# Performance work log

Hardware: AMD Instinct MI355X
Metric: run time of the kernel (lower is better)

## Reference

```python
import jax, jax.numpy as jnp
import numpy as np

B, T, S, D, V = 8, 64, 512, 512, 50000


def setup_inputs() -> dict:
    key = jax.random.key(0)
    k1, k2, k3, k4, k5 = jax.random.split(key, 5)
    x = jax.random.normal(k1, (B, T, D), dtype=jnp.float32)
    attn_dist = jax.random.normal(k2, (B, T, S), dtype=jnp.float32)
    enc_batch_extend_vocab = jax.random.randint(k3, (B, S), 0, V, dtype=jnp.int64)
    W_proj = jax.random.normal(k4, (D, V), dtype=jnp.float32) * (1.0 / np.sqrt(D))
    b_proj = jnp.zeros((V,), dtype=jnp.float32)
    W_pgen = jax.random.normal(k5, (D, 1), dtype=jnp.float32) * (1.0 / np.sqrt(D))
    b_pgen = jnp.zeros((1,), dtype=jnp.float32)
    return {"x": x, "attn_dist": attn_dist,
            "enc_batch_extend_vocab": enc_batch_extend_vocab,
            "W_proj": W_proj, "b_proj": b_proj,
            "W_pgen": W_pgen, "b_pgen": b_pgen}


def reference(x, attn_dist, enc_batch_extend_vocab, W_proj, b_proj, W_pgen, b_pgen):
    # pointer-generator head, temp=1, beam_search=False
    temp = 1.0
    # p_gen gate: [B, T, 1]
    alpha = jax.nn.sigmoid(jnp.einsum('btd,de->bte', x, W_pgen) + b_pgen)
    # vocab projection + softmax: [B, T, V]
    logit = jnp.einsum('btd,dv->btv', x, W_proj) + b_proj
    vocab_dist = jax.nn.softmax(logit / temp, axis=2)
    vocab_dist_ = alpha * vocab_dist
    # copy distribution over source positions: [B, T, S]
    attn = jax.nn.softmax(attn_dist / temp, axis=-1)
    attn_ = (1.0 - alpha) * attn
    # scatter_add copy probs into vocab dim (index broadcast over T)
    b_idx = jnp.arange(B)[:, None, None]        # [B,1,1]
    t_idx = jnp.arange(T)[None, :, None]        # [1,T,1]
    v_idx = enc_batch_extend_vocab[:, None, :]  # [B,1,S]
    merged = vocab_dist_.at[b_idx, t_idx, v_idx].add(attn_)
    return jnp.log(merged)
```

## Files before the change

### kernel.cpp

```cpp
#include <hip/hip_runtime.h>
#include <math.h>
#include <stdint.h>

#define B_ 8
#define T_ 64
#define S_ 512
#define D_ 512
#define V_ 50000
#define VP_ 50176
#define M_ (B_*T_)
#define ROWB_ ((size_t)V_ * 4)

typedef __bf16 bf16_t;
typedef bf16_t bf16x8 __attribute__((ext_vector_type(8)));
typedef float  f32x4  __attribute__((ext_vector_type(4)));

__device__ inline float blk_sum(float v, float* sm) {
    #pragma unroll
    for (int o = 32; o > 0; o >>= 1) v += __shfl_down(v, o);
    int lane = threadIdx.x & 63, wid = threadIdx.x >> 6;
    __syncthreads();
    if (lane == 0) sm[wid] = v;
    __syncthreads();
    return sm[0] + sm[1] + sm[2] + sm[3];
}

__device__ inline float blk_max(float v, float* sm) {
    #pragma unroll
    for (int o = 32; o > 0; o >>= 1) v = fmaxf(v, __shfl_down(v, o));
    int lane = threadIdx.x & 63, wid = threadIdx.x >> 6;
    __syncthreads();
    if (lane == 0) sm[wid] = v;
    __syncthreads();
    return fmaxf(fmaxf(sm[0], sm[1]), fmaxf(sm[2], sm[3]));
}

__device__ inline void unpack8(uint4 u, float f[8]) {
    uint32_t w0 = u.x, w1 = u.y, w2 = u.z, w3 = u.w;
    f[0] = __uint_as_float(w0 << 16); f[1] = __uint_as_float(w0 & 0xffff0000u);
    f[2] = __uint_as_float(w1 << 16); f[3] = __uint_as_float(w1 & 0xffff0000u);
    f[4] = __uint_as_float(w2 << 16); f[5] = __uint_as_float(w2 & 0xffff0000u);
    f[6] = __uint_as_float(w3 << 16); f[7] = __uint_as_float(w3 & 0xffff0000u);
}

__global__ __launch_bounds__(256) void k1_alpha_attn(
    const float* __restrict__ x, const float* __restrict__ attn_dist,
    const float* __restrict__ W_pgen, const float* __restrict__ b_pgen,
    float* __restrict__ logalpha_out, float* __restrict__ attn_out, bf16_t* __restrict__ xb)
{
    __shared__ float sm[4];
    int row = blockIdx.x;
    int tid = threadIdx.x;

    float2 xv = reinterpret_cast<const float2*>(x + (size_t)row * D_)[tid];
    float2 wv = reinterpret_cast<const float2*>(W_pgen)[tid];
    union { bf16_t h[2]; uint32_t u; } pk;
    pk.h[0] = (bf16_t)xv.x; pk.h[1] = (bf16_t)xv.y;
    reinterpret_cast<uint32_t*>(xb + (size_t)row * D_)[tid] = pk.u;

    float dot = blk_sum(xv.x * wv.x + xv.y * wv.y, sm);
    float alpha = 1.f / (1.f + expf(-(dot + b_pgen[0])));
    if (tid == 0) logalpha_out[row] = logf(alpha);

    float a0 = attn_dist[(size_t)row * S_ + tid];
    float a1 = attn_dist[(size_t)row * S_ + tid + 256];
    float mx = blk_max(fmaxf(a0, a1), sm);
    float e0 = expf(a0 - mx), e1 = expf(a1 - mx);
    float s = blk_sum(e0 + e1, sm);
    float scale = (1.f - alpha) / s;
    attn_out[(size_t)row * S_ + tid]       = e0 * scale;
    attn_out[(size_t)row * S_ + tid + 256] = e1 * scale;
}

__global__ __launch_bounds__(256) void conv_wt(const float* __restrict__ W, bf16_t* __restrict__ Wt)
{
    __shared__ float tile[64][65];
    int v0 = blockIdx.x * 64;
    int k0 = blockIdx.y * 64;
    int tid = threadIdx.x;
    #pragma unroll
    for (int p = 0; p < 4; p++) {
        int kl = (tid >> 4) + p * 16;
        int v  = v0 + (tid & 15) * 4;
        float4 val = make_float4(0.f, 0.f, 0.f, 0.f);
        if (v < V_)
            val = *reinterpret_cast<const float4*>(&W[(size_t)(k0 + kl) * V_ + v]);
        tile[kl][(tid & 15) * 4 + 0] = val.x;
        tile[kl][(tid & 15) * 4 + 1] = val.y;
        tile[kl][(tid & 15) * 4 + 2] = val.z;
        tile[kl][(tid & 15) * 4 + 3] = val.w;
    }
    __syncthreads();
    #pragma unroll
    for (int p = 0; p < 2; p++) {
        int vl = (tid >> 3) + p * 32;
        int kc = (tid & 7) * 8;
        union { bf16_t h[8]; uint4 u; } pk;
        #pragma unroll
        for (int j = 0; j < 8; j++) pk.h[j] = (bf16_t)tile[kc + j][vl];
        *reinterpret_cast<uint4*>(&Wt[(size_t)(v0 + vl) * D_ + k0 + kc]) = pk.u;
    }
}

#define GBM 128
#define GBN 128
#define GBK 32

__global__ __launch_bounds__(256) void k2_mfma(
    const bf16_t* __restrict__ A, const bf16_t* __restrict__ Wt,
    const float* __restrict__ bias, char* __restrict__ outB)
{
    __shared__ bf16_t As[GBM][GBK];
    __shared__ bf16_t Bs[GBN][GBK];
    int tid  = threadIdx.x;
    int lane = tid & 63;
    int w    = tid >> 6;
    int wm   = w >> 1, wn = w & 1;
    int bn = blockIdx.x * GBN;
    int bm = blockIdx.y * GBM;

    f32x4 acc[4][4] = {};

    for (int k0 = 0; k0 < D_; k0 += GBK) {
        #pragma unroll
        for (int i = 0; i < 2; i++) {
            int e = (w * 2 + i) * 512 + lane * 8;
            int r = e >> 5, c = e & 31;
            const bf16_t* g = &A[(size_t)(bm + r) * D_ + k0 + c];
            __builtin_amdgcn_global_load_lds(
                (const __attribute__((address_space(1))) void*)g,
                (__attribute__((address_space(3))) void*)&As[(w * 2 + i) * 16][0],
                16, 0, 0);
        }
        #pragma unroll
        for (int i = 0; i < 2; i++) {
            int e = (w * 2 + i) * 512 + lane * 8;
            int n = e >> 5, c = e & 31;
            const bf16_t* g = &Wt[(size_t)(bn + n) * D_ + k0 + c];
            __builtin_amdgcn_global_load_lds(
                (const __attribute__((address_space(1))) void*)g,
                (__attribute__((address_space(3))) void*)&Bs[(w * 2 + i) * 16][0],
                16, 0, 0);
        }
        asm volatile("s_waitcnt vmcnt(0)" ::: "memory");
        __syncthreads();

        bf16x8 af[4], bfr[4];
        int kb = (lane >> 4) * 8;
        #pragma unroll
        for (int mi = 0; mi < 4; mi++)
            af[mi] = *reinterpret_cast<const bf16x8*>(&As[wm * 64 + mi * 16 + (lane & 15)][kb]);
        #pragma unroll
        for (int ni = 0; ni < 4; ni++)
            bfr[ni] = *reinterpret_cast<const bf16x8*>(&Bs[wn * 64 + ni * 16 + (lane & 15)][kb]);
        #pragma unroll
        for (int mi = 0; mi < 4; mi++)
            #pragma unroll
            for (int ni = 0; ni < 4; ni++)
                acc[mi][ni] = __builtin_amdgcn_mfma_f32_16x16x32_bf16(af[mi], bfr[ni], acc[mi][ni], 0, 0, 0);
        __syncthreads();
    }

    int cm = bm + wm * 64, cn = bn + wn * 64;
    #pragma unroll
    for (int ni = 0; ni < 4; ni++) {
        int n = cn + ni * 16 + (lane & 15);
        float bv = (n < V_) ? bias[n] : 0.f;
        #pragma unroll
        for (int mi = 0; mi < 4; mi++) {
            int rbase = cm + mi * 16 + (lane >> 4) * 4;
            #pragma unroll
            for (int r = 0; r < 4; r++) {
                bf16_t val = (bf16_t)(acc[mi][ni][r] + bv);
                *reinterpret_cast<bf16_t*>(outB + (size_t)(rbase + r) * ROWB_ + 2 * (size_t)n) = val;
            }
        }
    }
}

__global__ __launch_bounds__(512) void k5a_owner(const int* __restrict__ idx, int* __restrict__ owner_g)
{
    __shared__ int ids[S_];
    int b = blockIdx.x;
    int s = threadIdx.x;
    ids[s] = idx[b * S_ + s];
    __syncthreads();
    int v = ids[s], o = s;
    for (int s2 = 0; s2 < s; s2++) if (ids[s2] == v) { o = s2; break; }
    owner_g[b * S_ + s] = o;
}

#define CHUNK_ 2048
#define NCH_ ((V_ + CHUNK_ - 1) / CHUNK_)

__global__ __launch_bounds__(256) void k345_final(
    char* __restrict__ outB, const float* __restrict__ attn_, const int* __restrict__ idx,
    const int* __restrict__ owner_g, const float* __restrict__ logalpha)
{
    __shared__ float att[S_];
    __shared__ int own[S_], ids[S_];
    __shared__ float smm[4], sms[4];
    int row = blockIdx.x;
    int b = row >> 6;
    int tid = threadIdx.x;
    int lane = tid & 63, wid = tid >> 6;

    for (int s = tid; s < S_; s += 256) {
        att[s] = attn_[(size_t)row * S_ + s];
        own[s] = owner_g[b * S_ + s];
        ids[s] = idx[b * S_ + s];
    }

    const uint4* L4 = reinterpret_cast<const uint4*>(outB + (size_t)row * ROWB_);
    float m = -INFINITY, se = 0.f;
    for (int i = tid; i < V_ / 8; i += 256) {
        uint4 u = L4[i];
        float f[8]; unpack8(u, f);
        float m8 = fmaxf(fmaxf(fmaxf(f[0], f[1]), fmaxf(f[2], f[3])),
                         fmaxf(fmaxf(f[4], f[5]), fmaxf(f[6], f[7])));
        float mn = fmaxf(m, m8);
        se = se * __expf(m - mn)
           + __expf(f[0] - mn) + __expf(f[1] - mn) + __expf(f[2] - mn) + __expf(f[3] - mn)
           + __expf(f[4] - mn) + __expf(f[5] - mn) + __expf(f[6] - mn) + __expf(f[7] - mn);
        m = mn;
    }
    #pragma unroll
    for (int o = 32; o > 0; o >>= 1) {
        float m2 = __shfl_down(m, o);
        float s2 = __shfl_down(se, o);
        float mn = fmaxf(m, m2);
        if (mn == -INFINITY) { se = 0.f; }
        else se = se * __expf(m - mn) + s2 * __expf(m2 - mn);
        m = mn;
    }
    __syncthreads();
    if (lane == 0) { smm[wid] = m; sms[wid] = se; }
    __syncthreads();
    float M = smm[0], Ssum = sms[0];
    #pragma unroll
    for (int wv = 1; wv < 4; wv++) {
        float m2 = smm[wv], s2 = sms[wv];
        float mn = fmaxf(M, m2);
        if (mn != -INFINITY) Ssum = Ssum * __expf(M - mn) + s2 * __expf(m2 - mn);
        M = mn;
    }
    float logden = M + logf(Ssum);
    float c_ = logalpha[row] - logden;

    for (int s = tid; s < S_; s += 256)
        if (own[s] != s) atomicAdd(&att[own[s]], att[s]);
    __syncthreads();

    const ushort* Lrow = reinterpret_cast<const ushort*>(outB + (size_t)row * ROWB_);
    float* frow = reinterpret_cast<float*>(outB + (size_t)row * ROWB_);
    for (int c = NCH_ - 1; c >= 0; c--) {
        int i0 = c * CHUNK_ + tid * 8;
        uint4 u = make_uint4(0, 0, 0, 0);
        bool act = (i0 + 8 <= V_);
        if (act) u = *reinterpret_cast<const uint4*>(Lrow + i0);
        __syncthreads();
        if (act) {
            float f[8]; unpack8(u, f);
            float4 lo = make_float4(f[0] + c_, f[1] + c_, f[2] + c_, f[3] + c_);
            float4 hi = make_float4(f[4] + c_, f[5] + c_, f[6] + c_, f[7] + c_);
            *reinterpret_cast<float4*>(frow + i0)     = lo;
            *reinterpret_cast<float4*>(frow + i0 + 4) = hi;
        }
        __syncthreads();
    }

    for (int s = tid; s < S_; s += 256) {
        if (own[s] == s) {
            int v = ids[s];
            frow[v] = logf(expf(frow[v]) + att[s]);
        }
    }
}

#define BM 64
#define BN 64
#define BK 16
__global__ __launch_bounds__(256) void k2_gemm(
    const float* __restrict__ A, const float* __restrict__ W,
    const float* __restrict__ bias, float* __restrict__ C)
{
    __shared__ float As2[BK][BM + 1];
    __shared__ float Bs2[BK][BN + 1];
    int bn = blockIdx.x * BN;
    int bm = blockIdx.y * BM;
    int tid = threadIdx.x;
    int tx = tid & 15;
    int ty = tid >> 4;
    bool full_n = (bn + BN <= V_);
    float acc[4][4] = {};
    for (int k0 = 0; k0 < D_; k0 += BK) {
        {
            int i = tid * 4;
            int row = i >> 4, col = i & 15;
            const float4 av = *reinterpret_cast<const float4*>(&A[(size_t)(bm + row) * D_ + k0 + col]);
            As2[col + 0][row] = av.x; As2[col + 1][row] = av.y;
            As2[col + 2][row] = av.z; As2[col + 3][row] = av.w;
        }
        {
            int i = tid * 4;
            int row = i >> 6, col = i & 63;
            int gn = bn + col;
            if (full_n) {
                const float4 bv = *reinterpret_cast<const float4*>(&W[(size_t)(k0 + row) * V_ + gn]);
                Bs2[row][col + 0] = bv.x; Bs2[row][col + 1] = bv.y;
                Bs2[row][col + 2] = bv.z; Bs2[row][col + 3] = bv.w;
            } else {
                #pragma unroll
                for (int j = 0; j < 4; j++)
                    Bs2[row][col + j] = (gn + j < V_) ? W[(size_t)(k0 + row) * V_ + gn + j] : 0.f;
            }
        }
        __syncthreads();
        #pragma unroll
        for (int kk = 0; kk < BK; kk++) {
            float a[4], b[4];
            #pragma unroll
            for (int i = 0; i < 4; i++) a[i] = As2[kk][ty * 4 + i];
            #pragma unroll
            for (int j = 0; j < 4; j++) b[j] = Bs2[kk][tx + j * 16];
            #pragma unroll
            for (int i = 0; i < 4; i++)
                #pragma unroll
                for (int j = 0; j < 4; j++)
                    acc[i][j] += a[i] * b[j];
        }
        __syncthreads();
    }
    #pragma unroll
    for (int i = 0; i < 4; i++) {
        int m = bm + ty * 4 + i;
        #pragma unroll
        for (int j = 0; j < 4; j++) {
            int n = bn + tx + j * 16;
            if (n < V_) C[(size_t)m * V_ + n] = acc[i][j] + bias[n];
        }
    }
}

__global__ __launch_bounds__(256) void k3_stats(const float* __restrict__ C, float* __restrict__ logden)
{
    __shared__ float smm[4], sms[4];
    int row = blockIdx.x;
    const float4* p = reinterpret_cast<const float4*>(C + (size_t)row * V_);
    float m = -INFINITY, s = 0.f;
    for (int i = threadIdx.x; i < V_ / 4; i += 256) {
        float4 v = p[i];
        float m4 = fmaxf(fmaxf(v.x, v.y), fmaxf(v.z, v.w));
        if (m4 > m) { s *= expf(m - m4); m = m4; }
        s += expf(v.x - m) + expf(v.y - m) + expf(v.z - m) + expf(v.w - m);
    }
    #pragma unroll
    for (int o = 32; o > 0; o >>= 1) {
        float m2 = __shfl_down(m, o);
        float s2 = __shfl_down(s, o);
        float mn = fmaxf(m, m2);
        s = s * expf(m - mn) + s2 * expf(m2 - mn);
        m = mn;
    }
    int lane = threadIdx.x & 63, wid = threadIdx.x >> 6;
    if (lane == 0) { smm[wid] = m; sms[wid] = s; }
    __syncthreads();
    if (threadIdx.x == 0) {
        float M = smm[0], S = sms[0];
        #pragma unroll
        for (int wv = 1; wv < 4; wv++) {
            float m2 = smm[wv], s2 = sms[wv];
            float mn = fmaxf(M, m2);
            S = S * expf(M - mn) + s2 * expf(m2 - mn);
            M = mn;
        }
        logden[row] = M + logf(S);
    }
}

__global__ __launch_bounds__(256) void k4_scale(
    float* __restrict__ C, const float* __restrict__ logalpha, const float* __restrict__ logden)
{
    int row = blockIdx.y;
    int i = blockIdx.x * 256 + threadIdx.x;
    if (i >= V_ / 4) return;
    float c_ = logalpha[row] - logden[row];
    float4* p = reinterpret_cast<float4*>(C + (size_t)row * V_) + i;
    float4 v = *p;
    v.x += c_; v.y += c_; v.z += c_; v.w += c_;
    *p = v;
}

__global__ __launch_bounds__(256) void k5_scatter_log(
    float* __restrict__ C, const float* __restrict__ attn_, const int* __restrict__ idx,
    const int* __restrict__ owner_g)
{
    __shared__ float att[S_];
    __shared__ int own[S_], ids[S_];
    int row = blockIdx.x;
    int b = row >> 6;
    int tid = threadIdx.x;
    for (int s = tid; s < S_; s += 256) {
        att[s] = attn_[(size_t)row * S_ + s];
        own[s] = owner_g[b * S_ + s];
        ids[s] = idx[b * S_ + s];
    }
    __syncthreads();
    for (int s = tid; s < S_; s += 256)
        if (own[s] != s) atomicAdd(&att[own[s]], att[s]);
    __syncthreads();
    for (int s = tid; s < S_; s += 256) {
        if (own[s] == s) {
            int v = ids[s];
            float* p = &C[(size_t)row * V_ + v];
            *p = logf(expf(*p) + att[s]);
        }
    }
}

extern "C" void kernel_launch(void* const* d_in, const int* in_sizes, int n_in,
                              void* d_out, int out_size, void* d_ws, size_t ws_size,
                              hipStream_t stream) {
    const float* x         = (const float*)d_in[0];
    const float* attn_dist = (const float*)d_in[1];
    const int*   ebev      = (const int*)  d_in[2];
    const float* W_proj    = (const float*)d_in[3];
    const float* b_proj    = (const float*)d_in[4];
    const float* W_pgen    = (const float*)d_in[5];
    const float* b_pgen    = (const float*)d_in[6];
    float* out = (float*)d_out;
    char*  outB = (char*)d_out;

    float*  logalpha = (float*)d_ws;
    float*  logden   = logalpha + M_;
    float*  attn_    = logden + M_;
    int*    owner    = (int*)(attn_ + (size_t)B_ * T_ * S_);
    bf16_t* xb       = (bf16_t*)(owner + (size_t)B_ * S_);
    bf16_t* Wt       = xb + (size_t)M_ * D_;
    size_t need = (size_t)(2 * M_ + B_ * T_ * S_ + B_ * S_) * 4
                + (size_t)M_ * D_ * 2 + (size_t)VP_ * D_ * 2;

    k1_alpha_attn<<<M_, 256, 0, stream>>>(x, attn_dist, W_pgen, b_pgen, logalpha, attn_, xb);
    k5a_owner<<<B_, 512, 0, stream>>>(ebev, owner);

    if (ws_size >= need) {
        dim3 gt(VP_ / 64, D_ / 64);
        conv_wt<<<gt, 256, 0, stream>>>(W_proj, Wt);

        dim3 g2(VP_ / GBN, M_ / GBM);
        k2_mfma<<<g2, 256, 0, stream>>>(xb, Wt, b_proj, outB);

        k345_final<<<M_, 256, 0, stream>>>(outB, attn_, ebev, owner, logalpha);
    } else {
        dim3 g2((V_ + BN - 1) / BN, M_ / BM);
        k2_gemm<<<g2, 256, 0, stream>>>(x, W_proj, b_proj, out);
        k3_stats<<<M_, 256, 0, stream>>>(out, logden);
        dim3 g4((V_ / 4 + 255) / 256, M_);
        k4_scale<<<g4, 256, 0, stream>>>(out, logalpha, logden);
        k5_scatter_log<<<M_, 256, 0, stream>>>(out, attn_, ebev, owner);
    }
}
```

Measured before the change: 172.1 us.

## Merge prep kernels into one launch and double-buffer MFMA GEMM LDS tiles

Three preprocessing kernels (weight transpose/convert to bf16, alpha/attention softmax with x conversion, and the duplicate-index owner computation) are merged into one launch that dispatches work by block index. This removes two launch gaps and lets the small tasks run alongside the large conversion. The bf16 MFMA GEMM now uses two LDS buffers, issuing the next k-tile's global-to-LDS loads before computing the current tile, so the sync per k-step overlaps load latency with MFMA work. LDS use doubles and the owner loop now runs over 256 threads with two iterations each.

```diff
diff --git a/kernel.cpp b/kernel.cpp
--- a/kernel.cpp
+++ b/kernel.cpp
@@ -43,75 +43,90 @@
     f[6] = __uint_as_float(w3 << 16); f[7] = __uint_as_float(w3 & 0xffff0000u);
 }
 
-__global__ __launch_bounds__(256) void k1_alpha_attn(
+#define CONVB_ (784 * 8)
+
+__global__ __launch_bounds__(256) void kprep(
+    const float* __restrict__ W, bf16_t* __restrict__ Wt,
     const float* __restrict__ x, const float* __restrict__ attn_dist,
     const float* __restrict__ W_pgen, const float* __restrict__ b_pgen,
-    float* __restrict__ logalpha_out, float* __restrict__ attn_out, bf16_t* __restrict__ xb)
-{
-    __shared__ float sm[4];
-    int row = blockIdx.x;
+    float* __restrict__ logalpha_out, float* __restrict__ attn_out, bf16_t* __restrict__ xb,
+    const int* __restrict__ idx, int* __restrict__ owner_g)
+{
+    __shared__ float tile[64][65];
+    int bid = blockIdx.x;
     int tid = threadIdx.x;
 
-    float2 xv = reinterpret_cast<const float2*>(x + (size_t)row * D_)[tid];
-    float2 wv = reinterpret_cast<const float2*>(W_pgen)[tid];
-    union { bf16_t h[2]; uint32_t u; } pk;
-    pk.h[0] = (bf16_t)xv.x; pk.h[1] = (bf16_t)xv.y;
-    reinterpret_cast<uint32_t*>(xb + (size_t)row * D_)[tid] = pk.u;
-
-    float dot = blk_sum(xv.x * wv.x + xv.y * wv.y, sm);
-    float alpha = 1.f / (1.f + expf(-(dot + b_pgen[0])));
-    if (tid == 0) logalpha_out[row] = logf(alpha);
-
-    float a0 = attn_dist[(size_t)row * S_ + tid];
-    float a1 = attn_dist[(size_t)row * S_ + tid + 256];
-    float mx = blk_max(fmaxf(a0, a1), sm);
-    float e0 = expf(a0 - mx), e1 = expf(a1 - mx);
-    float s = blk_sum(e0 + e1, sm);
-    float scale = (1.f - alpha) / s;
-    attn_out[(size_t)row * S_ + tid]       = e0 * scale;
-    attn_out[(size_t)row * S_ + tid + 256] = e1 * scale;
-}
-
-__global__ __launch_bounds__(256) void conv_wt(const float* __restrict__ W, bf16_t* __restrict__ Wt)
-{
-    __shared__ float tile[64][65];
-    int v0 = blockIdx.x * 64;
-    int k0 = blockIdx.y * 64;
-    int tid = threadIdx.x;
-    #pragma unroll
-    for (int p = 0; p < 4; p++) {
-        int kl = (tid >> 4) + p * 16;
-        int v  = v0 + (tid & 15) * 4;
-        float4 val = make_float4(0.f, 0.f, 0.f, 0.f);
-        if (v < V_)
-            val = *reinterpret_cast<const float4*>(&W[(size_t)(k0 + kl) * V_ + v]);
-        tile[kl][(tid & 15) * 4 + 0] = val.x;
-        tile[kl][(tid & 15) * 4 + 1] = val.y;
-        tile[kl][(tid & 15) * 4 + 2] = val.z;
-        tile[kl][(tid & 15) * 4 + 3] = val.w;
-    }
-    __syncthreads();
-    #pragma unroll
-    for (int p = 0; p < 2; p++) {
-        int vl = (tid >> 3) + p * 32;
-        int kc = (tid & 7) * 8;
-        union { bf16_t h[8]; uint4 u; } pk;
+    if (bid < CONVB_) {
+        int v0 = (bid % 784) * 64;
+        int k0 = (bid / 784) * 64;
         #pragma unroll
-        for (int j = 0; j < 8; j++) pk.h[j] = (bf16_t)tile[kc + j][vl];
-        *reinterpret_cast<uint4*>(&Wt[(size_t)(v0 + vl) * D_ + k0 + kc]) = pk.u;
+        for (int p = 0; p < 4; p++) {
+            int kl = (tid >> 4) + p * 16;
+            int v  = v0 + (tid & 15) * 4;
+            float4 val = make_float4(0.f, 0.f, 0.f, 0.f);
+            if (v < V_)
+                val = *reinterpret_cast<const float4*>(&W[(size_t)(k0 + kl) * V_ + v]);
+            tile[kl][(tid & 15) * 4 + 0] = val.x;
+            tile[kl][(tid & 15) * 4 + 1] = val.y;
+            tile[kl][(tid & 15) * 4 + 2] = val.z;
+            tile[kl][(tid & 15) * 4 + 3] = val.w;
+        }
+        __syncthreads();
+        #pragma unroll
+        for (int p = 0; p < 2; p++) {
+            int vl = (tid >> 3) + p * 32;
+            int kc = (tid & 7) * 8;
+            union { bf16_t h[8]; uint4 u; } pk;
+            #pragma unroll
+            for (int j = 0; j < 8; j++) pk.h[j] = (bf16_t)tile[kc + j][vl];
+            *reinterpret_cast<uint4*>(&Wt[(size_t)(v0 + vl) * D_ + k0 + kc]) = pk.u;
+        }
+    } else if (bid < CONVB_ + M_) {
+        float* sm = &tile[0][0];
+        int row = bid - CONVB_;
+
+        float2 xv = reinterpret_cast<const float2*>(x + (size_t)row * D_)[tid];
+        float2 wv = reinterpret_cast<const float2*>(W_pgen)[tid];
+        union { bf16_t h[2]; uint32_t u; } pk;
+        pk.h[0] = (bf16_t)xv.x; pk.h[1] = (bf16_t)xv.y;
+        reinterpret_cast<uint32_t*>(xb + (size_t)row * D_)[tid] = pk.u;
+
+        float dot = blk_sum(xv.x * wv.x + xv.y * wv.y, sm);
+        float alpha = 1.f / (1.f + expf(-(dot + b_pgen[0])));
+        if (tid == 0) logalpha_out[row] = logf(alpha);
+
+        float a0 = attn_dist[(size_t)row * S_ + tid];
+        float a1 = attn_dist[(size_t)row * S_ + tid + 256];
+        float mx = blk_max(fmaxf(a0, a1), sm);
+        float e0 = expf(a0 - mx), e1 = expf(a1 - mx);
+        float s = blk_sum(e0 + e1, sm);
+        float scale = (1.f - alpha) / s;
+        attn_out[(size_t)row * S_ + tid]       = e0 * scale;
+        attn_out[(size_t)row * S_ + tid + 256] = e1 * scale;
+    } else {
+        int* ids = reinterpret_cast<int*>(&tile[0][0]);
+        int b = bid - (CONVB_ + M_);
+        for (int s = tid; s < S_; s += 256) ids[s] = idx[b * S_ + s];
+        __syncthreads();
+        for (int s = tid; s < S_; s += 256) {
+            int v = ids[s], o = s;
+            for (int s2 = 0; s2 < s; s2++) if (ids[s2] == v) { o = s2; break; }
+            owner_g[b * S_ + s] = o;
+        }
     }
 }
 
 #define GBM 128
 #define GBN 128
 #define GBK 32
+#define NT2_ (D_/GBK)
 
 __global__ __launch_bounds__(256) void k2_mfma(
     const bf16_t* __restrict__ A, const bf16_t* __restrict__ Wt,
     const float* __restrict__ bias, char* __restrict__ outB)
 {
-    __shared__ bf16_t As[GBM][GBK];
-    __shared__ bf16_t Bs[GBN][GBK];
+    __shared__ bf16_t As0[GBM][GBK], As1[GBM][GBK];
+    __shared__ bf16_t Bs0[GBN][GBK], Bs1[GBN][GBK];
     int tid  = threadIdx.x;
     int lane = tid & 63;
     int w    = tid >> 6;
@@ -121,45 +136,60 @@
 
     f32x4 acc[4][4] = {};
 
-    for (int k0 = 0; k0 < D_; k0 += GBK) {
-        #pragma unroll
-        for (int i = 0; i < 2; i++) {
-            int e = (w * 2 + i) * 512 + lane * 8;
-            int r = e >> 5, c = e & 31;
-            const bf16_t* g = &A[(size_t)(bm + r) * D_ + k0 + c];
-            __builtin_amdgcn_global_load_lds(
-                (const __attribute__((address_space(1))) void*)g,
-                (__attribute__((address_space(3))) void*)&As[(w * 2 + i) * 16][0],
-                16, 0, 0);
-        }
-        #pragma unroll
-        for (int i = 0; i < 2; i++) {
-            int e = (w * 2 + i) * 512 + lane * 8;
-            int n = e >> 5, c = e & 31;
-            const bf16_t* g = &Wt[(size_t)(bn + n) * D_ + k0 + c];
-            __builtin_amdgcn_global_load_lds(
-                (const __attribute__((address_space(1))) void*)g,
-                (__attribute__((address_space(3))) void*)&Bs[(w * 2 + i) * 16][0],
-                16, 0, 0);
-        }
+#define STAGE(dstA, dstB, k0)                                                          \
+    {                                                                                  \
+        _Pragma("unroll")                                                              \
+        for (int i = 0; i < 2; i++) {                                                  \
+            int e = (w * 2 + i) * 512 + lane * 8;                                      \
+            int r = e >> 5, c = e & 31;                                                \
+            __builtin_amdgcn_global_load_lds(                                          \
+                (const __attribute__((address_space(1))) void*)                        \
+                    &A[(size_t)(bm + r) * D_ + (k0) + c],                              \
+                (__attribute__((address_space(3))) void*)&dstA[(w * 2 + i) * 16][0],   \
+                16, 0, 0);                                                             \
+            __builtin_amdgcn_global_load_lds(                                          \
+                (const __attribute__((address_space(1))) void*)                        \
+                    &Wt[(size_t)(bn + r) * D_ + (k0) + c],                             \
+                (__attribute__((address_space(3))) void*)&dstB[(w * 2 + i) * 16][0],   \
+                16, 0, 0);                                                             \
+        }                                                                              \
+    }
+
+#define COMPUTE(srcA, srcB)                                                            \
+    {                                                                                  \
+        bf16x8 af[4], bfr[4];                                                          \
+        int kb = (lane >> 4) * 8;                                                      \
+        _Pragma("unroll")                                                              \
+        for (int mi = 0; mi < 4; mi++)                                                 \
+            af[mi] = *reinterpret_cast<const bf16x8*>(&srcA[wm * 64 + mi * 16 + (lane & 15)][kb]); \
+        _Pragma("unroll")                                                              \
+        for (int ni = 0; ni < 4; ni++)                                                 \
+            bfr[ni] = *reinterpret_cast<const bf16x8*>(&srcB[wn * 64 + ni * 16 + (lane & 15)][kb]); \
+        _Pragma("unroll")                                                              \
+        for (int mi = 0; mi < 4; mi++)                                                 \
+            _Pragma("unroll")                                                          \
+            for (int ni = 0; ni < 4; ni++)                                             \
+                acc[mi][ni] = __builtin_amdgcn_mfma_f32_16x16x32_bf16(af[mi], bfr[ni], acc[mi][ni], 0, 0, 0); \
+    }
+
+    STAGE(As0, Bs0, 0);
+    asm volatile("s_waitcnt vmcnt(0)" ::: "memory");
+    __syncthreads();
+
+    #pragma unroll
+    for (int tt = 0; tt < NT2_ / 2; tt++) {
+        int k0 = tt * 2 * GBK;
+        if (k0 + GBK < D_) STAGE(As1, Bs1, k0 + GBK);
+        COMPUTE(As0, Bs0);
         asm volatile("s_waitcnt vmcnt(0)" ::: "memory");
         __syncthreads();
-
-        bf16x8 af[4], bfr[4];
-        int kb = (lane >> 4) * 8;
-        #pragma unroll
-        for (int mi = 0; mi < 4; mi++)
-            af[mi] = *reinterpret_cast<const bf16x8*>(&As[wm * 64 + mi * 16 + (lane & 15)][kb]);
-        #pragma unroll
-        for (int ni = 0; ni < 4; ni++)
-            bfr[ni] = *reinterpret_cast<const bf16x8*>(&Bs[wn * 64 + ni * 16 + (lane & 15)][kb]);
-        #pragma unroll
-        for (int mi = 0; mi < 4; mi++)
-            #pragma unroll
-            for (int ni = 0; ni < 4; ni++)
-                acc[mi][ni] = __builtin_amdgcn_mfma_f32_16x16x32_bf16(af[mi], bfr[ni], acc[mi][ni], 0, 0, 0);
-        __syncthreads();
-    }
+        if (k0 + 2 * GBK < D_) STAGE(As0, Bs0, k0 + 2 * GBK);
+        COMPUTE(As1, Bs1);
+        asm volatile("s_waitcnt vmcnt(0)" ::: "memory");
+        __syncthreads();
+    }
+#undef STAGE
+#undef COMPUTE
 
     int cm = bm + wm * 64, cn = bn + wn * 64;
     #pragma unroll
@@ -176,18 +206,6 @@
             }
         }
     }
-}
-
-__global__ __launch_bounds__(512) void k5a_owner(const int* __restrict__ idx, int* __restrict__ owner_g)
-{
-    __shared__ int ids[S_];
-    int b = blockIdx.x;
-    int s = threadIdx.x;
-    ids[s] = idx[b * S_ + s];
-    __syncthreads();
-    int v = ids[s], o = s;
-    for (int s2 = 0; s2 < s; s2++) if (ids[s2] == v) { o = s2; break; }
-    owner_g[b * S_ + s] = o;
 }
 
 #define CHUNK_ 2048
@@ -275,6 +293,41 @@
             frow[v] = logf(expf(frow[v]) + att[s]);
         }
     }
+}
+
+__global__ __launch_bounds__(256) void k1_alpha_attn(
+    const float* __restrict__ x, const float* __restrict__ attn_dist,
+    const float* __restrict__ W_pgen, const float* __restrict__ b_pgen,
+    float* __restrict__ logalpha_out, float* __restrict__ attn_out)
+{
+    __shared__ float sm[4];
+    int row = blockIdx.x;
+    int tid = threadIdx.x;
+    float2 xv = reinterpret_cast<const float2*>(x + (size_t)row * D_)[tid];
+    float2 wv = reinterpret_cast<const float2*>(W_pgen)[tid];
+    float dot = blk_sum(xv.x * wv.x + xv.y * wv.y, sm);
+    float alpha = 1.f / (1.f + expf(-(dot + b_pgen[0])));
+    if (tid == 0) logalpha_out[row] = logf(alpha);
+    float a0 = attn_dist[(size_t)row * S_ + tid];
+    float a1 = attn_dist[(size_t)row * S_ + tid + 256];
+    float mx = blk_max(fmaxf(a0, a1), sm);
+    float e0 = expf(a0 - mx), e1 = expf(a1 - mx);
+    float s = blk_sum(e0 + e1, sm);
+    float scale = (1.f - alpha) / s;
+    attn_out[(size_t)row * S_ + tid]       = e0 * scale;
+    attn_out[(size_t)row * S_ + tid + 256] = e1 * scale;
+}
+
+__global__ __launch_bounds__(512) void k5a_owner(const int* __restrict__ idx, int* __restrict__ owner_g)
+{
+    __shared__ int ids[S_];
+    int b = blockIdx.x;
+    int s = threadIdx.x;
+    ids[s] = idx[b * S_ + s];
+    __syncthreads();
+    int v = ids[s], o = s;
+    for (int s2 = 0; s2 < s; s2++) if (ids[s2] == v) { o = s2; break; }
+    owner_g[b * S_ + s] = o;
 }
 
 #define BM 64
@@ -440,18 +493,17 @@
     size_t need = (size_t)(2 * M_ + B_ * T_ * S_ + B_ * S_) * 4
                 + (size_t)M_ * D_ * 2 + (size_t)VP_ * D_ * 2;
 
-    k1_alpha_attn<<<M_, 256, 0, stream>>>(x, attn_dist, W_pgen, b_pgen, logalpha, attn_, xb);
-    k5a_owner<<<B_, 512, 0, stream>>>(ebev, owner);
-
     if (ws_size >= need) {
-        dim3 gt(VP_ / 64, D_ / 64);
-        conv_wt<<<gt, 256, 0, stream>>>(W_proj, Wt);
+        kprep<<<CONVB_ + M_ + B_, 256, 0, stream>>>(
+            W_proj, Wt, x, attn_dist, W_pgen, b_pgen, logalpha, attn_, xb, ebev, owner);
 
         dim3 g2(VP_ / GBN, M_ / GBM);
         k2_mfma<<<g2, 256, 0, stream>>>(xb, Wt, b_proj, outB);
 
         k345_final<<<M_, 256, 0, stream>>>(outB, attn_, ebev, owner, logalpha);
     } else {
+        k1_alpha_attn<<<M_, 256, 0, stream>>>(x, attn_dist, W_pgen, b_pgen, logalpha, attn_);
+        k5a_owner<<<B_, 512, 0, stream>>>(ebev, owner);
         dim3 g2((V_ + BN - 1) / BN, M_ / BM);
         k2_gemm<<<g2, 256, 0, stream>>>(x, W_proj, b_proj, out);
         k3_stats<<<M_, 256, 0, stream>>>(out, logden);
```

Result: faster. 157.4 us (-8.6%).
